# Performance work log

Hardware: AMD Instinct MI355X
Metric: run time of the kernel (lower is better)

The kernel has to match this reference:

```python
import jax, jax.numpy as jnp
import numpy as np

N_NODES, N_EDGES, D, N_RELS = 50000, 600000, 128, 460


def setup_inputs() -> dict:
    key = jax.random.key(0)
    ks = jax.random.split(key, 8)
    h = jax.random.normal(ks[0], (N_NODES, D), dtype=jnp.float32)
    emb_rel = jax.random.normal(ks[1], (N_RELS, D), dtype=jnp.float32)
    attn_fc_w = jax.random.normal(ks[2], (D, 3 * D), dtype=jnp.float32) * 0.05   # Linear(3D->D), weight [out,in]
    attn_fc2_w = jax.random.normal(ks[3], (1, D), dtype=jnp.float32) * 0.05     # Linear(D->1)
    loop_weight = jax.random.normal(ks[4], (D, D), dtype=jnp.float32) * 0.05
    edge_src = jax.random.randint(ks[5], (N_EDGES,), 0, N_NODES)
    edge_dst = jax.random.randint(ks[6], (N_EDGES,), 0, N_NODES)
    edge_type = jax.random.randint(ks[7], (N_EDGES,), 0, N_RELS)
    return {"h": h, "emb_rel": emb_rel, "attn_fc_w": attn_fc_w,
            "attn_fc2_w": attn_fc2_w, "loop_weight": loop_weight,
            "edge_src": edge_src, "edge_dst": edge_dst, "edge_type": edge_type}


def reference(h, emb_rel, attn_fc_w, attn_fc2_w, loop_weight, edge_src, edge_dst, edge_type):
    n = h.shape[0]
    # --- per-edge gather ---
    hs = h[edge_src]            # [E, D] src features (mailbox 'e_h')
    ht = h[edge_dst]            # [E, D]
    rel = emb_rel[edge_type]    # [E, D]
    # --- concat-MLP attention: leaky_relu(fc2(fc1([hs|ht|rel]))) ---
    z2 = jnp.concatenate([hs, ht, rel], axis=1)          # [E, 3D]
    a = z2 @ attn_fc_w.T                                  # [E, D]
    e = jax.nn.leaky_relu(a @ attn_fc2_w.T)               # [E, 1], slope 0.01 (torch default)
    # --- per-destination segment softmax ---
    m = jax.ops.segment_max(e, edge_dst, num_segments=n)  # [N, 1]
    m = jnp.where(jnp.isfinite(m), m, jnp.float32(0.0))   # empty nodes -> -inf; neutralize
    ex = jnp.exp(e - m[edge_dst])                         # [E, 1]
    den = jax.ops.segment_sum(ex, edge_dst, num_segments=n)
    alpha = ex / den[edge_dst]                            # [E, 1]
    # --- weighted scatter-sum of src features ---
    node_repr = jax.ops.segment_sum(alpha * hs, edge_dst, num_segments=n)  # [N, D]
    # --- self-loop ---
    node_repr = node_repr + h @ loop_weight
    return node_repr
```

## Files before the change

### kernel.cpp

```cpp
#include <hip/hip_runtime.h>

#define N_NODES 50000
#define N_EDGES 600000
#define D 128
#define N_RELS 460
#define CAP_LOG 6

typedef unsigned short u16;
typedef __attribute__((ext_vector_type(8))) short bf16x8;
typedef __attribute__((ext_vector_type(4))) float f32x4;

enum : int {
    OFF_W      = 0,
    OFF_S1     = 384,
    OFF_S2     = 50384,
    OFF_S3     = 100384,
    OFF_COUNTS = 100864,
    OFF_CSR    = 900864,
    OFF_HB     = 4100864,
};

#define GEMM_BLOCKS  782
#define ZERO_BLOCKS  196
#define W_BLOCKS     2
#define FILL_BLOCKS  293
#define REL_WAVES    115
#define REL_BLOCKS   29
#define WT_STRIDE    136

__device__ __forceinline__ float blo(unsigned u) { return __uint_as_float(u << 16); }
__device__ __forceinline__ float bhi(unsigned u) { return __uint_as_float(u & 0xFFFF0000u); }

__device__ __forceinline__ unsigned cvtpk(float lo, float hi) {
    unsigned d;
    asm("v_cvt_pk_bf16_f32 %0, %1, %2" : "=v"(d) : "v"(lo), "v"(hi));
    return d;
}

__global__ __launch_bounds__(256) void k_init(
        int* __restrict__ counts,
        const float* __restrict__ fc1, const float* __restrict__ fc2,
        float* __restrict__ w) {
    int t = threadIdx.x;
    if (blockIdx.x < ZERO_BLOCKS) {
        int i4 = blockIdx.x * 256 + t;
        #pragma unroll
        for (int rep = 0; rep < 4; ++rep) {
            int idx = i4 * 4 + rep;
            if (idx * 4 < N_NODES * 16)
                ((int4*)counts)[idx] = make_int4(0, 0, 0, 0);
        }
    } else {
        int j = (blockIdx.x - ZERO_BLOCKS) * 256 + t;
        if (j < 3 * D) {
            float acc = 0.f;
            #pragma unroll 8
            for (int k = 0; k < D; ++k) acc += fc2[k] * fc1[k * 3 * D + j];
            w[j] = acc;
        }
    }
}

__global__ __launch_bounds__(256) void k_prep(
        const int* __restrict__ src, const int* __restrict__ dst,
        const int* __restrict__ typ, int* __restrict__ counts,
        unsigned* __restrict__ csr,
        const float* __restrict__ loopw, const float* __restrict__ h,
        const float* __restrict__ w, const float* __restrict__ emb_rel,
        u16* __restrict__ hb, float* __restrict__ out,
        float* __restrict__ s1, float* __restrict__ s2, float* __restrict__ s3) {
    int t = threadIdx.x;
    if (blockIdx.x < FILL_BLOCKS) {
        int i = blockIdx.x * blockDim.x + t;
        if (i >= N_EDGES / 8) return;
        int4 da = ((const int4*)dst)[2 * i],     db = ((const int4*)dst)[2 * i + 1];
        int4 sa = ((const int4*)src)[2 * i],     sb = ((const int4*)src)[2 * i + 1];
        int4 ta = ((const int4*)typ)[2 * i],     tb = ((const int4*)typ)[2 * i + 1];
        int l0 = atomicAdd(&counts[da.x << 4], 1);
        int l1 = atomicAdd(&counts[da.y << 4], 1);
        int l2 = atomicAdd(&counts[da.z << 4], 1);
        int l3 = atomicAdd(&counts[da.w << 4], 1);
        int l4 = atomicAdd(&counts[db.x << 4], 1);
        int l5 = atomicAdd(&counts[db.y << 4], 1);
        int l6 = atomicAdd(&counts[db.z << 4], 1);
        int l7 = atomicAdd(&counts[db.w << 4], 1);
        csr[(da.x << CAP_LOG) + l0] = (unsigned)sa.x | ((unsigned)ta.x << 16);
        csr[(da.y << CAP_LOG) + l1] = (unsigned)sa.y | ((unsigned)ta.y << 16);
        csr[(da.z << CAP_LOG) + l2] = (unsigned)sa.z | ((unsigned)ta.z << 16);
        csr[(da.w << CAP_LOG) + l3] = (unsigned)sa.w | ((unsigned)ta.w << 16);
        csr[(db.x << CAP_LOG) + l4] = (unsigned)sb.x | ((unsigned)tb.x << 16);
        csr[(db.y << CAP_LOG) + l5] = (unsigned)sb.y | ((unsigned)tb.y << 16);
        csr[(db.z << CAP_LOG) + l6] = (unsigned)sb.z | ((unsigned)tb.z << 16);
        csr[(db.w << CAP_LOG) + l7] = (unsigned)sb.w | ((unsigned)tb.w << 16);
    } else if (blockIdx.x < FILL_BLOCKS + GEMM_BLOCKS) {
        int gb = blockIdx.x - FILL_BLOCKS;
        __shared__ u16 Ws[(D + 16) * WT_STRIDE];
        for (int u = t; u < 512; u += 256) {
            int ko = u >> 5, nq = u & 31;
            const float* wp = loopw + (size_t)ko * 8 * D + nq * 4;
            float v[4][8];
            #pragma unroll
            for (int r = 0; r < 8; ++r) {
                float4 f = *(const float4*)(wp + (size_t)r * D);
                v[0][r] = f.x; v[1][r] = f.y; v[2][r] = f.z; v[3][r] = f.w;
            }
            #pragma unroll
            for (int c = 0; c < 4; ++c) {
                union { bf16x8 b; unsigned q[4]; } pk;
                #pragma unroll
                for (int p = 0; p < 4; ++p)
                    pk.q[p] = cvtpk(v[c][2 * p], v[c][2 * p + 1]);
                *(bf16x8*)&Ws[(nq * 4 + c) * WT_STRIDE + ko * 8] = pk.b;
            }
        }
        {
            int row = 128 + (t >> 4);
            int k8  = (t & 15) * 8;
            union { bf16x8 b; unsigned q[4]; } pk;
            if (row == 128) {
                #pragma unroll
                for (int p = 0; p < 4; ++p)
                    pk.q[p] = cvtpk(w[k8 + 2 * p], w[k8 + 2 * p + 1]);
            } else if (row == 129) {
                #pragma unroll
                for (int p = 0; p < 4; ++p)
                    pk.q[p] = cvtpk(w[D + k8 + 2 * p], w[D + k8 + 2 * p + 1]);
            } else {
                #pragma unroll
                for (int p = 0; p < 4; ++p) pk.q[p] = 0u;
            }
            *(bf16x8*)&Ws[row * WT_STRIDE + k8] = pk.b;
        }
        __syncthreads();

        int wave = t >> 6, lane = t & 63;
        int quad = lane >> 4, m16 = lane & 15;
        int nbase = gb * 64 + wave * 16;

        f32x4 acc[9];
        #pragma unroll
        for (int cg = 0; cg < 9; ++cg) acc[cg] = (f32x4){0.f, 0.f, 0.f, 0.f};

        int arow = nbase + m16;
        if (arow >= N_NODES) arow = N_NODES - 1;
        const float* aptr = h + (size_t)arow * D + quad * 8;
        u16* hbp = hb + (size_t)arow * D + quad * 8;

        #pragma unroll
        for (int k0 = 0; k0 < D; k0 += 32) {
            float4 a0 = *(const float4*)(aptr + k0);
            float4 a1 = *(const float4*)(aptr + k0 + 4);
            union { bf16x8 b; unsigned q[4]; } A;
            A.q[0] = cvtpk(a0.x, a0.y);
            A.q[1] = cvtpk(a0.z, a0.w);
            A.q[2] = cvtpk(a1.x, a1.y);
            A.q[3] = cvtpk(a1.z, a1.w);
            *(bf16x8*)(hbp + k0) = A.b;
            #pragma unroll
            for (int cg = 0; cg < 9; ++cg) {
                bf16x8 bb = *(const bf16x8*)(&Ws[(cg * 16 + m16) * WT_STRIDE + k0 + quad * 8]);
                acc[cg] = __builtin_amdgcn_mfma_f32_16x16x32_bf16(A.b, bb, acc[cg], 0, 0, 0);
            }
        }
        #pragma unroll
        for (int reg = 0; reg < 4; ++reg) {
            int row = nbase + quad * 4 + reg;
            if (row < N_NODES) {
                #pragma unroll
                for (int cg = 0; cg < 8; ++cg)
                    out[(size_t)row * D + cg * 16 + m16] = acc[cg][reg];
            }
        }
        if (m16 < 2) {
            float* sp = (m16 == 0) ? s1 : s2;
            #pragma unroll
            for (int reg = 0; reg < 4; ++reg) {
                int row = nbase + quad * 4 + reg;
                if (row < N_NODES) sp[row] = acc[8][reg];
            }
        }
    } else {
        int wv = ((blockIdx.x - FILL_BLOCKS - GEMM_BLOCKS) * 256 + t) >> 6;
        if (wv >= REL_WAVES) return;
        int l   = t & 63;
        int sub = l >> 4;
        int q   = l & 15;
        int r = wv * 4 + sub;
        const float* rp = emb_rel + (size_t)r * D + q * 8;
        float4 r0 = *(const float4*)rp;
        float4 r1 = *(const float4*)(rp + 4);
        float4 w30 = *(const float4*)(w + 2 * D + q * 8);
        float4 w31 = *(const float4*)(w + 2 * D + q * 8 + 4);
        float a3 = r0.x * w30.x + r0.y * w30.y + r0.z * w30.z + r0.w * w30.w
                 + r1.x * w31.x + r1.y * w31.y + r1.z * w31.z + r1.w * w31.w;
        #pragma unroll
        for (int o = 8; o; o >>= 1) a3 += __shfl_xor(a3, o, 16);
        if (q == 0) s3[r] = a3;
    }
}

#define ROWACC(uu, cc)                                                         \
    accA.x += (cc) * blo((uu).x);  accA.y += (cc) * bhi((uu).x);               \
    accA.z += (cc) * blo((uu).y);  accA.w += (cc) * bhi((uu).y);               \
    accB.x += (cc) * blo((uu).z);  accB.y += (cc) * bhi((uu).z);               \
    accB.z += (cc) * blo((uu).w);  accB.w += (cc) * bhi((uu).w);

__global__ void k_gather(const u16* __restrict__ hb, const int* __restrict__ counts,
                         const unsigned* __restrict__ csr,
                         const float* __restrict__ s1, const float* __restrict__ s2,
                         const float* __restrict__ s3, float* __restrict__ out) {
    int n  = (blockIdx.x * blockDim.x + threadIdx.x) >> 4;
    int gl = threadIdx.x & 15;
    if (n >= N_NODES) return;
    int deg = counts[n << 4];
    if (deg == 0) return;
    int beg = n << CAP_LOG;
    int end = beg + deg;

    float s2n = s2[n];
    float den = 0.f;
    f32x4 accA = {0.f, 0.f, 0.f, 0.f}, accB = {0.f, 0.f, 0.f, 0.f};

    for (int cb = beg; cb < end; cb += 16) {
        int i = cb + gl;
        int msrc = 0; float mex = 0.f;
        if (i < end) {
            unsigned p = csr[i];
            msrc = (int)(p & 0xFFFFu);
            float x = s1[msrc] + s2n + s3[p >> 16];
            float lv = (x > 0.f) ? x : 0.01f * x;
            mex = __expf(lv);
        }
        den += mex;
        int cnt  = min(16, end - cb);
        int cntr = (cnt + 3) & ~3;
        int j = 0;
        for (; j + 7 < cntr; j += 8) {
            int aa[8]; float cc[8]; uint4 uu[8];
            #pragma unroll
            for (int u = 0; u < 8; ++u) {
                aa[u] = __shfl(msrc, j + u, 16);
                cc[u] = __shfl(mex,  j + u, 16);
            }
            #pragma unroll
            for (int u = 0; u < 8; ++u)
                uu[u] = ((const uint4*)(hb + (size_t)aa[u] * D))[gl];
            #pragma unroll
            for (int u = 0; u < 8; ++u) { ROWACC(uu[u], cc[u]); }
        }
        for (; j < cntr; j += 4) {
            int aa[4]; float cc[4]; uint4 uu[4];
            #pragma unroll
            for (int u = 0; u < 4; ++u) {
                aa[u] = __shfl(msrc, j + u, 16);
                cc[u] = __shfl(mex,  j + u, 16);
            }
            #pragma unroll
            for (int u = 0; u < 4; ++u)
                uu[u] = ((const uint4*)(hb + (size_t)aa[u] * D))[gl];
            #pragma unroll
            for (int u = 0; u < 4; ++u) { ROWACC(uu[u], cc[u]); }
        }
    }
    #pragma unroll
    for (int o = 8; o; o >>= 1) den += __shfl_xor(den, o, 16);
    float inv = 1.f / den;

    f32x4* op = (f32x4*)(out + (size_t)n * D + gl * 8);
    f32x4 o0 = __builtin_nontemporal_load(op);
    f32x4 o1 = __builtin_nontemporal_load(op + 1);
    o0 += accA * inv;
    o1 += accB * inv;
    __builtin_nontemporal_store(o0, op);
    __builtin_nontemporal_store(o1, op + 1);
}

extern "C" void kernel_launch(void* const* d_in, const int* in_sizes, int n_in,
                              void* d_out, int out_size, void* d_ws, size_t ws_size,
                              hipStream_t stream) {
    const float* h       = (const float*)d_in[0];
    const float* emb_rel = (const float*)d_in[1];
    const float* fc1     = (const float*)d_in[2];
    const float* fc2     = (const float*)d_in[3];
    const float* loopw   = (const float*)d_in[4];
    const int*   esrc    = (const int*)d_in[5];
    const int*   edst    = (const int*)d_in[6];
    const int*   etyp    = (const int*)d_in[7];
    float* out = (float*)d_out;
    float* ws  = (float*)d_ws;

    float*    w       = ws + OFF_W;
    float*    s1      = ws + OFF_S1;
    float*    s2      = ws + OFF_S2;
    float*    s3      = ws + OFF_S3;
    int*      counts  = (int*)(ws + OFF_COUNTS);
    unsigned* csr     = (unsigned*)(ws + OFF_CSR);
    u16*      hb      = (u16*)(ws + OFF_HB);

    k_init<<<ZERO_BLOCKS + W_BLOCKS, 256, 0, stream>>>(counts, fc1, fc2, w);

    k_prep<<<FILL_BLOCKS + GEMM_BLOCKS + REL_BLOCKS, 256, 0, stream>>>(
        esrc, edst, etyp, counts, csr, loopw, h, w, emb_rel,
        hb, out, s1, s2, s3);

    k_gather<<<(N_NODES * 16 + 255) / 256, 256, 0, stream>>>(
        hb, counts, csr, s1, s2, s3, out);
}
```

Measured before the change: 159.1 us.

## Stage GEMM outputs through LDS for coalesced stores and compact degree counters

The self-loop GEMM now writes its fp32 output tile and the bf16 copy of h through shared memory, so each goes to global memory as contiguous row-wise vector stores instead of strided per-lane scalar or fragment stores. The bf16 staging uses an XOR swizzle to avoid LDS bank conflicts. Separately, the per-node degree counters are packed densely instead of padded to 64-byte strides, which shrinks the zeroing work and the counter footprint but may increase atomic contention on shared cache lines. The staging adds several block barriers and LDS round-trips.

Measured after the change: 161.6 us. About the same (+1.6%).

```diff
diff --git a/kernel.cpp b/kernel.cpp
--- a/kernel.cpp
+++ b/kernel.cpp
@@ -21,12 +21,13 @@
 };
 
 #define GEMM_BLOCKS  782
-#define ZERO_BLOCKS  196
+#define ZERO_BLOCKS  13
 #define W_BLOCKS     2
 #define FILL_BLOCKS  293
 #define REL_WAVES    115
 #define REL_BLOCKS   29
 #define WT_STRIDE    136
+#define OT_STRIDE    136
 
 __device__ __forceinline__ float blo(unsigned u) { return __uint_as_float(u << 16); }
 __device__ __forceinline__ float bhi(unsigned u) { return __uint_as_float(u & 0xFFFF0000u); }
@@ -47,7 +48,7 @@
         #pragma unroll
         for (int rep = 0; rep < 4; ++rep) {
             int idx = i4 * 4 + rep;
-            if (idx * 4 < N_NODES * 16)
+            if (idx < N_NODES / 4)
                 ((int4*)counts)[idx] = make_int4(0, 0, 0, 0);
         }
     } else {
@@ -76,14 +77,14 @@
         int4 da = ((const int4*)dst)[2 * i],     db = ((const int4*)dst)[2 * i + 1];
         int4 sa = ((const int4*)src)[2 * i],     sb = ((const int4*)src)[2 * i + 1];
         int4 ta = ((const int4*)typ)[2 * i],     tb = ((const int4*)typ)[2 * i + 1];
-        int l0 = atomicAdd(&counts[da.x << 4], 1);
-        int l1 = atomicAdd(&counts[da.y << 4], 1);
-        int l2 = atomicAdd(&counts[da.z << 4], 1);
-        int l3 = atomicAdd(&counts[da.w << 4], 1);
-        int l4 = atomicAdd(&counts[db.x << 4], 1);
-        int l5 = atomicAdd(&counts[db.y << 4], 1);
-        int l6 = atomicAdd(&counts[db.z << 4], 1);
-        int l7 = atomicAdd(&counts[db.w << 4], 1);
+        int l0 = atomicAdd(&counts[da.x], 1);
+        int l1 = atomicAdd(&counts[da.y], 1);
+        int l2 = atomicAdd(&counts[da.z], 1);
+        int l3 = atomicAdd(&counts[da.w], 1);
+        int l4 = atomicAdd(&counts[db.x], 1);
+        int l5 = atomicAdd(&counts[db.y], 1);
+        int l6 = atomicAdd(&counts[db.z], 1);
+        int l7 = atomicAdd(&counts[db.w], 1);
         csr[(da.x << CAP_LOG) + l0] = (unsigned)sa.x | ((unsigned)ta.x << 16);
         csr[(da.y << CAP_LOG) + l1] = (unsigned)sa.y | ((unsigned)ta.y << 16);
         csr[(da.z << CAP_LOG) + l2] = (unsigned)sa.z | ((unsigned)ta.z << 16);
@@ -94,7 +95,8 @@
         csr[(db.w << CAP_LOG) + l7] = (unsigned)sb.w | ((unsigned)tb.w << 16);
     } else if (blockIdx.x < FILL_BLOCKS + GEMM_BLOCKS) {
         int gb = blockIdx.x - FILL_BLOCKS;
-        __shared__ u16 Ws[(D + 16) * WT_STRIDE];
+        __shared__ __align__(16) char smem[(D + 16) * WT_STRIDE * 2];
+        u16* Ws = (u16*)smem;
         for (int u = t; u < 512; u += 256) {
             int ko = u >> 5, nq = u & 31;
             const float* wp = loopw + (size_t)ko * 8 * D + nq * 4;
@@ -144,10 +146,11 @@
         int arow = nbase + m16;
         if (arow >= N_NODES) arow = N_NODES - 1;
         const float* aptr = h + (size_t)arow * D + quad * 8;
-        u16* hbp = hb + (size_t)arow * D + quad * 8;
-
-        #pragma unroll
-        for (int k0 = 0; k0 < D; k0 += 32) {
+
+        bf16x8 afr[4];
+        #pragma unroll
+        for (int s = 0; s < 4; ++s) {
+            int k0 = s * 32;
             float4 a0 = *(const float4*)(aptr + k0);
             float4 a1 = *(const float4*)(aptr + k0 + 4);
             union { bf16x8 b; unsigned q[4]; } A;
@@ -155,28 +158,63 @@
             A.q[1] = cvtpk(a0.z, a0.w);
             A.q[2] = cvtpk(a1.x, a1.y);
             A.q[3] = cvtpk(a1.z, a1.w);
-            *(bf16x8*)(hbp + k0) = A.b;
+            afr[s] = A.b;
             #pragma unroll
             for (int cg = 0; cg < 9; ++cg) {
                 bf16x8 bb = *(const bf16x8*)(&Ws[(cg * 16 + m16) * WT_STRIDE + k0 + quad * 8]);
                 acc[cg] = __builtin_amdgcn_mfma_f32_16x16x32_bf16(A.b, bb, acc[cg], 0, 0, 0);
             }
         }
-        #pragma unroll
-        for (int reg = 0; reg < 4; ++reg) {
-            int row = nbase + quad * 4 + reg;
-            if (row < N_NODES) {
-                #pragma unroll
-                for (int cg = 0; cg < 8; ++cg)
-                    out[(size_t)row * D + cg * 16 + m16] = acc[cg][reg];
-            }
-        }
+
         if (m16 < 2) {
             float* sp = (m16 == 0) ? s1 : s2;
             #pragma unroll
             for (int reg = 0; reg < 4; ++reg) {
                 int row = nbase + quad * 4 + reg;
                 if (row < N_NODES) sp[row] = acc[8][reg];
+            }
+        }
+
+        __syncthreads();
+        float* ot = (float*)smem;
+        #pragma unroll
+        for (int cg = 0; cg < 8; ++cg)
+            #pragma unroll
+            for (int reg = 0; reg < 4; ++reg)
+                ot[(wave * 16 + quad * 4 + reg) * OT_STRIDE + cg * 16 + m16] = acc[cg][reg];
+        __syncthreads();
+        {
+            int rowbase = gb * 64;
+            #pragma unroll
+            for (int rep = 0; rep < 8; ++rep) {
+                int i = rep * 256 + t;
+                int r = i >> 5, c4 = i & 31;
+                if (rowbase + r < N_NODES) {
+                    float4 v = *(const float4*)&ot[r * OT_STRIDE + c4 * 4];
+                    ((float4*)out)[(size_t)(rowbase + r) * 32 + c4] = v;
+                }
+            }
+        }
+
+        __syncthreads();
+        u16* at = (u16*)smem;
+        #pragma unroll
+        for (int s = 0; s < 4; ++s) {
+            int chunk = (s * 4 + quad) ^ (m16 & 7);
+            *(bf16x8*)&at[(wave * 16 + m16) * 136 + chunk * 8] = afr[s];
+        }
+        __syncthreads();
+        {
+            int rowbase = gb * 64;
+            #pragma unroll
+            for (int rep = 0; rep < 4; ++rep) {
+                int i = rep * 256 + t;
+                int r = i >> 4, c8 = i & 15;
+                if (rowbase + r < N_NODES) {
+                    int chunk = c8 ^ (r & 7);
+                    bf16x8 v = *(const bf16x8*)&at[r * 136 + chunk * 8];
+                    *(bf16x8*)(hb + (size_t)(rowbase + r) * D + c8 * 8) = v;
+                }
             }
         }
     } else {
@@ -212,7 +250,7 @@
     int n  = (blockIdx.x * blockDim.x + threadIdx.x) >> 4;
     int gl = threadIdx.x & 15;
     if (n >= N_NODES) return;
-    int deg = counts[n << 4];
+    int deg = counts[n];
     if (deg == 0) return;
     int beg = n << CAP_LOG;
     int end = beg + deg;
```

## Compact degree counters and compute edge weights redundantly per lane in gather

Applied to the files above, without the earlier changes.

Degree counters are packed densely instead of padded to 64-byte strides, so the zeroing pass shrinks and the count reads become contiguous. In the gather kernel every lane of the 16-lane group now loads all 16 CSR entries as vectors and computes the attention scores and exps itself. This removes the cross-lane shuffles and the final denominator reduction. The output row load is hoisted ahead of the loop to overlap its latency. The trade-offs are 16x redundant score computation and s1/s3 lookups per lane, and more atomic contention on shared cache lines for the counters.

Measured after the change: 166.0 us. 4.4% more time.

```diff
diff --git a/kernel.cpp b/kernel.cpp
--- a/kernel.cpp
+++ b/kernel.cpp
@@ -21,7 +21,7 @@
 };
 
 #define GEMM_BLOCKS  782
-#define ZERO_BLOCKS  196
+#define ZERO_BLOCKS  13
 #define W_BLOCKS     2
 #define FILL_BLOCKS  293
 #define REL_WAVES    115
@@ -47,7 +47,7 @@
         #pragma unroll
         for (int rep = 0; rep < 4; ++rep) {
             int idx = i4 * 4 + rep;
-            if (idx * 4 < N_NODES * 16)
+            if (idx < N_NODES / 4)
                 ((int4*)counts)[idx] = make_int4(0, 0, 0, 0);
         }
     } else {
@@ -76,14 +76,14 @@
         int4 da = ((const int4*)dst)[2 * i],     db = ((const int4*)dst)[2 * i + 1];
         int4 sa = ((const int4*)src)[2 * i],     sb = ((const int4*)src)[2 * i + 1];
         int4 ta = ((const int4*)typ)[2 * i],     tb = ((const int4*)typ)[2 * i + 1];
-        int l0 = atomicAdd(&counts[da.x << 4], 1);
-        int l1 = atomicAdd(&counts[da.y << 4], 1);
-        int l2 = atomicAdd(&counts[da.z << 4], 1);
-        int l3 = atomicAdd(&counts[da.w << 4], 1);
-        int l4 = atomicAdd(&counts[db.x << 4], 1);
-        int l5 = atomicAdd(&counts[db.y << 4], 1);
-        int l6 = atomicAdd(&counts[db.z << 4], 1);
-        int l7 = atomicAdd(&counts[db.w << 4], 1);
+        int l0 = atomicAdd(&counts[da.x], 1);
+        int l1 = atomicAdd(&counts[da.y], 1);
+        int l2 = atomicAdd(&counts[da.z], 1);
+        int l3 = atomicAdd(&counts[da.w], 1);
+        int l4 = atomicAdd(&counts[db.x], 1);
+        int l5 = atomicAdd(&counts[db.y], 1);
+        int l6 = atomicAdd(&counts[db.z], 1);
+        int l7 = atomicAdd(&counts[db.w], 1);
         csr[(da.x << CAP_LOG) + l0] = (unsigned)sa.x | ((unsigned)ta.x << 16);
         csr[(da.y << CAP_LOG) + l1] = (unsigned)sa.y | ((unsigned)ta.y << 16);
         csr[(da.z << CAP_LOG) + l2] = (unsigned)sa.z | ((unsigned)ta.z << 16);
@@ -212,63 +212,55 @@
     int n  = (blockIdx.x * blockDim.x + threadIdx.x) >> 4;
     int gl = threadIdx.x & 15;
     if (n >= N_NODES) return;
-    int deg = counts[n << 4];
+    int deg = counts[n];
     if (deg == 0) return;
+
+    f32x4* op = (f32x4*)(out + (size_t)n * D + gl * 8);
+    f32x4 o0 = __builtin_nontemporal_load(op);
+    f32x4 o1 = __builtin_nontemporal_load(op + 1);
+
     int beg = n << CAP_LOG;
     int end = beg + deg;
-
     float s2n = s2[n];
     float den = 0.f;
     f32x4 accA = {0.f, 0.f, 0.f, 0.f}, accB = {0.f, 0.f, 0.f, 0.f};
 
     for (int cb = beg; cb < end; cb += 16) {
-        int i = cb + gl;
-        int msrc = 0; float mex = 0.f;
-        if (i < end) {
-            unsigned p = csr[i];
-            msrc = (int)(p & 0xFFFFu);
-            float x = s1[msrc] + s2n + s3[p >> 16];
+        int rem = end - cb;
+        const uint4* cw = (const uint4*)(csr + cb);
+        uint4 c0 = cw[0], c1 = cw[1], c2 = cw[2], c3 = cw[3];
+        unsigned cp[16] = { c0.x, c0.y, c0.z, c0.w,  c1.x, c1.y, c1.z, c1.w,
+                            c2.x, c2.y, c2.z, c2.w,  c3.x, c3.y, c3.z, c3.w };
+        int   ms[16];
+        float ex[16];
+        #pragma unroll
+        for (int j = 0; j < 16; ++j) {
+            unsigned p = cp[j];
+            int m = (int)(p & 0xFFFFu);
+            float x = s1[m] + s2n + s3[p >> 16];
             float lv = (x > 0.f) ? x : 0.01f * x;
-            mex = __expf(lv);
-        }
-        den += mex;
-        int cnt  = min(16, end - cb);
-        int cntr = (cnt + 3) & ~3;
-        int j = 0;
-        for (; j + 7 < cntr; j += 8) {
-            int aa[8]; float cc[8]; uint4 uu[8];
-            #pragma unroll
-            for (int u = 0; u < 8; ++u) {
-                aa[u] = __shfl(msrc, j + u, 16);
-                cc[u] = __shfl(mex,  j + u, 16);
-            }
-            #pragma unroll
-            for (int u = 0; u < 8; ++u)
-                uu[u] = ((const uint4*)(hb + (size_t)aa[u] * D))[gl];
-            #pragma unroll
-            for (int u = 0; u < 8; ++u) { ROWACC(uu[u], cc[u]); }
-        }
-        for (; j < cntr; j += 4) {
-            int aa[4]; float cc[4]; uint4 uu[4];
-            #pragma unroll
-            for (int u = 0; u < 4; ++u) {
-                aa[u] = __shfl(msrc, j + u, 16);
-                cc[u] = __shfl(mex,  j + u, 16);
-            }
-            #pragma unroll
-            for (int u = 0; u < 4; ++u)
-                uu[u] = ((const uint4*)(hb + (size_t)aa[u] * D))[gl];
-            #pragma unroll
-            for (int u = 0; u < 4; ++u) { ROWACC(uu[u], cc[u]); }
+            float e = __expf(lv);
+            bool ok = j < rem;
+            ms[j] = ok ? m : 0;
+            ex[j] = ok ? e : 0.f;
+            den += ex[j];
+        }
+        #pragma unroll
+        for (int b = 0; b < 2; ++b) {
+            if (b * 8 < rem) {
+                uint4 uu[8];
+                #pragma unroll
+                for (int u = 0; u < 8; ++u)
+                    uu[u] = ((const uint4*)(hb + (size_t)ms[b * 8 + u] * D))[gl];
+                #pragma unroll
+                for (int u = 0; u < 8; ++u) {
+                    float cc = ex[b * 8 + u];
+                    ROWACC(uu[u], cc);
+                }
+            }
         }
     }
-    #pragma unroll
-    for (int o = 8; o; o >>= 1) den += __shfl_xor(den, o, 16);
     float inv = 1.f / den;
-
-    f32x4* op = (f32x4*)(out + (size_t)n * D + gl * 8);
-    f32x4 o0 = __builtin_nontemporal_load(op);
-    f32x4 o1 = __builtin_nontemporal_load(op + 1);
     o0 += accA * inv;
     o1 += accB * inv;
     __builtin_nontemporal_store(o0, op);
```
